# Kernel tuning notes

Measured on AMD Instinct MI355X. Metric: run time of the kernel, lower is better.

Reference implementation:

```python
import jax, jax.numpy as jnp
import numpy as np

ALPHA = 0.95  # membrane/filter decay
BETA = 0.9    # output decay
NB_HIDDEN, NB_OUTPUTS, NB_STEPS, BATCH = 256, 16, 2000, 128


def setup_inputs() -> dict:
    key = jax.random.key(0)
    k1, k2 = jax.random.split(key)
    inputs = jax.random.normal(k1, (BATCH, NB_STEPS, NB_HIDDEN), dtype=jnp.float32)
    weight_scale = 0.2
    output_weights = jax.random.normal(k2, (NB_HIDDEN, NB_OUTPUTS), dtype=jnp.float32) * (
        weight_scale / np.sqrt(NB_HIDDEN)
    )
    return {"inputs": inputs, "output_weights": output_weights}


def reference(inputs, output_weights):
    # inputs: [B, T, H], output_weights: [H, O]
    h2 = jnp.einsum("bth,ho->bto", inputs, output_weights)  # [B, T, O]
    B, T, O = h2.shape
    dtype = h2.dtype

    def step(carry, h_t):
        flt, out = carry
        new_flt = ALPHA * flt + h_t        # uses old flt
        new_out = BETA * out + flt         # uses OLD flt (matches torch code)
        return (new_flt, new_out), new_out

    init = (jnp.zeros((B, O), dtype), jnp.zeros((B, O), dtype))
    _, outs = jax.lax.scan(step, init, jnp.swapaxes(h2, 0, 1))  # outs: [T, B, O]
    out_rec = jnp.concatenate(
        [jnp.zeros((B, 1, O), dtype), jnp.swapaxes(outs, 0, 1)], axis=1
    )  # [B, T+1, O], first slot is the initial zero state (out_rec = [out0] + ...)
    return out_rec
```

## Files before the change

kernel.cpp:

```cpp
#include <hip/hip_runtime.h>


constexpr int B_ = 128, T_ = 2000, H_ = 256, O_ = 16;
constexpr int TOUT = T_ + 1;
constexpr int TC = 8, CL = 250;
constexpr int NHC = 16, HC = 16;
constexpr int BUFSLOTS = 1024;
constexpr int PAD = 20;
constexpr float ALPHA = 0.95f, BETA = 0.9f;
constexpr float INV_AB = 20.0f;
constexpr float L2A = -0.07400058144377693f;
constexpr float L2B = -0.15200309344504997f;

#define AS1 __attribute__((address_space(1)))
#define AS3 __attribute__((address_space(3)))

__device__ __forceinline__ void gload16(const float* g, float* l) {
    __builtin_amdgcn_global_load_lds((const AS1 void*)g, (AS3 void*)l, 16, 0, 0);
}

__device__ __forceinline__ void stage_chunk(const float* __restrict__ inb, int c,
                                            float* dst, int tid) {
#pragma unroll
    for (int it = 0; it < 4; ++it) {
        const int f = it * 256 + tid;
        int r = f >> 2;
        if (r > CL - 1) r = CL - 1;
        const int q = f & 3;
        const float* g = inb + (size_t)r * H_ + c * HC + 4 * (q ^ (r & 3));
        gload16(g, dst + (size_t)f * 4);
    }
}

__global__ __launch_bounds__(256, 4)
void h2scan_kernel(const float* __restrict__ in, const float* __restrict__ W,
                   float* __restrict__ out, float* __restrict__ ws) {
    __shared__ float lds[2 * BUFSLOTS * 4];
    const int tid = threadIdx.x;
    const int b = blockIdx.x >> 3;
    const int j = blockIdx.x & 7;

    const float* inb = in + ((size_t)b * T_ + (size_t)j * CL) * H_;
    const int row = (tid < CL) ? tid : 0;
    const int rsw = row & 3;

    float acc[16];
#pragma unroll
    for (int o = 0; o < 16; ++o) acc[o] = 0.f;

    stage_chunk(inb, 0, &lds[0], tid);
    __syncthreads();

    for (int c = 0; c < NHC; ++c) {
        float* cur = &lds[(c & 1) * (BUFSLOTS * 4)];
        if (c + 1 < NHC)
            stage_chunk(inb, c + 1, &lds[((c + 1) & 1) * (BUFSLOTS * 4)], tid);

        const float* __restrict__ Wc = W + c * HC * O_;
#pragma unroll
        for (int p = 0; p < 4; ++p) {
            const float4 v = *(const float4*)&cur[row * 16 + 4 * (p ^ rsw)];
            const float xv[4] = {v.x, v.y, v.z, v.w};
#pragma unroll
            for (int e = 0; e < 4; ++e) {
                const float x = xv[e];
                const float* wrow = Wc + (4 * p + e) * 16;
#pragma unroll
                for (int o = 0; o < 16; ++o)
                    acc[o] = fmaf(x, wrow[o], acc[o]);
            }
        }
        __syncthreads();
    }

    if (tid < CL) {
        float4* tp = (float4*)&lds[tid * PAD];
        tp[0] = make_float4(acc[0],  acc[1],  acc[2],  acc[3]);
        tp[1] = make_float4(acc[4],  acc[5],  acc[6],  acc[7]);
        tp[2] = make_float4(acc[8],  acc[9],  acc[10], acc[11]);
        tp[3] = make_float4(acc[12], acc[13], acc[14], acc[15]);
    }
    __syncthreads();

    if (tid < O_) {
        float flt = 0.f, oo = 0.f;
        float* col = &lds[tid];
#pragma unroll 5
        for (int t = 0; t < CL; ++t) {
            const float h = col[t * PAD];
            const float no = fmaf(BETA, oo, flt);
            flt = fmaf(ALPHA, flt, h);
            col[t * PAD] = no;
            oo = no;
        }
        float* wp = ws + ((size_t)(b * O_ + tid) * TC + j) * 2;
        wp[0] = flt;
        wp[1] = oo;
        if (j == 0) out[(size_t)b * TOUT * O_ + tid] = 0.f;
    }
    __syncthreads();

    float4* ob = (float4*)(out + ((size_t)b * TOUT + (size_t)j * CL + 1) * O_);
#pragma unroll
    for (int it = 0; it < 4; ++it) {
        const int e4 = it * 256 + tid;
        if (e4 < CL * 4) {
            const int tloc = e4 >> 2, qo = 4 * (e4 & 3);
            const float* tp = &lds[tloc * PAD + qo];
            ob[e4] = make_float4(tp[0], tp[1], tp[2], tp[3]);
        }
    }
}

__global__ __launch_bounds__(256)
void fixup_kernel(float* __restrict__ out, const float* __restrict__ ws) {
    const int blk = blockIdx.x;
    const int b = blk >> 3;
    const int j = blk & 7;
    if (j == 0) return;

    __shared__ float f0s[O_], o0s[O_];
    const int tid = threadIdx.x;
    if (tid < O_) {
        const float* wp = ws + ((size_t)(b * O_ + tid) * TC) * 2;
        float f = 0.f, oacc = 0.f;
        for (int m = 0; m < j; ++m) {
            const float k  = (float)((j - 1 - m) * CL);
            const float a  = exp2f(k * L2A);
            const float bb = exp2f(k * L2B);
            const float g  = (a - bb) * INV_AB;
            const float sf = wp[m * 2 + 0];
            const float so = wp[m * 2 + 1];
            f    = fmaf(a, sf, f);
            oacc = fmaf(g, sf, fmaf(bb, so, oacc));
        }
        f0s[tid] = f;
        o0s[tid] = oacc;
    }
    __syncthreads();

    float4* ob = (float4*)(out + ((size_t)b * TOUT + (size_t)j * CL + 1) * O_);
#pragma unroll
    for (int it = 0; it < 4; ++it) {
        const int e4 = it * 256 + tid;
        if (e4 < CL * 4) {
            const int tloc = e4 >> 2, qo = 4 * (e4 & 3);
            const float k  = (float)(tloc + 1);
            const float a  = exp2f(k * L2A);
            const float bb = exp2f(k * L2B);
            const float g  = (a - bb) * INV_AB;
            float4 v = ob[e4];
            v.x = fmaf(g, f0s[qo + 0], fmaf(bb, o0s[qo + 0], v.x));
            v.y = fmaf(g, f0s[qo + 1], fmaf(bb, o0s[qo + 1], v.y));
            v.z = fmaf(g, f0s[qo + 2], fmaf(bb, o0s[qo + 2], v.z));
            v.w = fmaf(g, f0s[qo + 3], fmaf(bb, o0s[qo + 3], v.w));
            ob[e4] = v;
        }
    }
}

extern "C" void kernel_launch(void* const* d_in, const int* in_sizes, int n_in,
                              void* d_out, int out_size, void* d_ws, size_t ws_size,
                              hipStream_t stream) {
    const float* in = (const float*)d_in[0];
    const float* W  = (const float*)d_in[1];
    float* out = (float*)d_out;
    float* ws  = (float*)d_ws;

    h2scan_kernel<<<dim3(B_ * TC), dim3(256), 0, stream>>>(in, W, out, ws);
    fixup_kernel<<<dim3(B_ * TC), dim3(256), 0, stream>>>(out, ws);
}
```

Before: 73.05 us.

## Make LDS staging wave-private and drop per-chunk block barriers

Each wave now stages only the input rows it consumes into its own LDS region. That lets the block-wide __syncthreads per H-chunk be replaced by manual s_waitcnt vmcnt/lgkmcnt waits. The two-buffer ring is primed two chunks ahead, and each buffer is refilled right after its data has been read into registers, so global loads overlap with the FMA work. The goal is to remove barrier stalls and let waves progress independently, at the cost of depending on hand-written waitcnt counts being correct.

```diff
diff --git a/kernel.cpp b/kernel.cpp
--- a/kernel.cpp
+++ b/kernel.cpp
@@ -5,7 +5,6 @@
 constexpr int TOUT = T_ + 1;
 constexpr int TC = 8, CL = 250;
 constexpr int NHC = 16, HC = 16;
-constexpr int BUFSLOTS = 1024;
 constexpr int PAD = 20;
 constexpr float ALPHA = 0.95f, BETA = 0.9f;
 constexpr float INV_AB = 20.0f;
@@ -19,59 +18,89 @@
     __builtin_amdgcn_global_load_lds((const AS1 void*)g, (AS3 void*)l, 16, 0, 0);
 }
 
-__device__ __forceinline__ void stage_chunk(const float* __restrict__ inb, int c,
-                                            float* dst, int tid) {
-#pragma unroll
-    for (int it = 0; it < 4; ++it) {
-        const int f = it * 256 + tid;
-        int r = f >> 2;
-        if (r > CL - 1) r = CL - 1;
-        const int q = f & 3;
-        const float* g = inb + (size_t)r * H_ + c * HC + 4 * (q ^ (r & 3));
-        gload16(g, dst + (size_t)f * 4);
-    }
-}
-
 __global__ __launch_bounds__(256, 4)
 void h2scan_kernel(const float* __restrict__ in, const float* __restrict__ W,
                    float* __restrict__ out, float* __restrict__ ws) {
-    __shared__ float lds[2 * BUFSLOTS * 4];
-    const int tid = threadIdx.x;
-    const int b = blockIdx.x >> 3;
-    const int j = blockIdx.x & 7;
+    __shared__ float lds[2 * 4096];
+    const int tid  = threadIdx.x;
+    const int w    = tid >> 6, lane = tid & 63;
+    const int b    = blockIdx.x >> 3;
+    const int j    = blockIdx.x & 7;
 
     const float* inb = in + ((size_t)b * T_ + (size_t)j * CL) * H_;
-    const int row = (tid < CL) ? tid : 0;
-    const int rsw = row & 3;
+    const int thrSlot = w * 256 + lane * 4;
+    const int rsw = lane & 3;
 
     float acc[16];
 #pragma unroll
     for (int o = 0; o < 16; ++o) acc[o] = 0.f;
 
-    stage_chunk(inb, 0, &lds[0], tid);
-    __syncthreads();
-
-    for (int c = 0; c < NHC; ++c) {
-        float* cur = &lds[(c & 1) * (BUFSLOTS * 4)];
-        if (c + 1 < NHC)
-            stage_chunk(inb, c + 1, &lds[((c + 1) & 1) * (BUFSLOTS * 4)], tid);
+    auto stage = [&](int c, int k) {
+#pragma unroll
+        for (int it = 0; it < 4; ++it) {
+            const int s = it * 64 + lane;
+            int r = w * 64 + (s >> 2);
+            if (r > CL - 1) r = CL - 1;
+            const int q = s & 3;
+            gload16(inb + (size_t)r * H_ + c * HC + 4 * (q ^ (r & 3)),
+                    &lds[(size_t)k * 4096 + (size_t)(w * 256 + s) * 4]);
+        }
+    };
+
+    stage(0, 0);
+    stage(1, 1);
+
+    for (int c = 0; c < NHC - 1; ++c) {
+        asm volatile("s_waitcnt vmcnt(4)" ::: "memory");
+        __builtin_amdgcn_sched_barrier(0);
+        const int k = c & 1;
+        float4 xv[4];
+#pragma unroll
+        for (int p = 0; p < 4; ++p)
+            xv[p] = *(const float4*)&lds[(size_t)k * 4096 +
+                                         (size_t)(thrSlot + (p ^ rsw)) * 4];
+        asm volatile("s_waitcnt lgkmcnt(0)" ::: "memory");
+        __builtin_amdgcn_sched_barrier(0);
+        if (c < NHC - 2) stage(c + 2, k);
 
         const float* __restrict__ Wc = W + c * HC * O_;
 #pragma unroll
         for (int p = 0; p < 4; ++p) {
-            const float4 v = *(const float4*)&cur[row * 16 + 4 * (p ^ rsw)];
-            const float xv[4] = {v.x, v.y, v.z, v.w};
+            const float xe[4] = {xv[p].x, xv[p].y, xv[p].z, xv[p].w};
 #pragma unroll
             for (int e = 0; e < 4; ++e) {
-                const float x = xv[e];
+                const float x = xe[e];
                 const float* wrow = Wc + (4 * p + e) * 16;
 #pragma unroll
                 for (int o = 0; o < 16; ++o)
                     acc[o] = fmaf(x, wrow[o], acc[o]);
             }
         }
-        __syncthreads();
-    }
+    }
+    {
+        asm volatile("s_waitcnt vmcnt(0)" ::: "memory");
+        __builtin_amdgcn_sched_barrier(0);
+        const int c = NHC - 1, k = c & 1;
+        float4 xv[4];
+#pragma unroll
+        for (int p = 0; p < 4; ++p)
+            xv[p] = *(const float4*)&lds[(size_t)k * 4096 +
+                                         (size_t)(thrSlot + (p ^ rsw)) * 4];
+        const float* __restrict__ Wc = W + c * HC * O_;
+#pragma unroll
+        for (int p = 0; p < 4; ++p) {
+            const float xe[4] = {xv[p].x, xv[p].y, xv[p].z, xv[p].w};
+#pragma unroll
+            for (int e = 0; e < 4; ++e) {
+                const float x = xe[e];
+                const float* wrow = Wc + (4 * p + e) * 16;
+#pragma unroll
+                for (int o = 0; o < 16; ++o)
+                    acc[o] = fmaf(x, wrow[o], acc[o]);
+            }
+        }
+    }
+    __syncthreads();
 
     if (tid < CL) {
         float4* tp = (float4*)&lds[tid * PAD];
```

Result: faster. 68.42 us (-6.3%).
